# Kernel tuning notes

Hardware: AMD Instinct MI355X
Metric: run time of the kernel (lower is better)

## Reference

```python
import jax, jax.numpy as jnp
import numpy as np

B, NN, BBX, CLS, LAT = 8192, 64, 6, 16, 128
IN = LAT + NN + CLS  # 208
NT = B * NN          # total nodes in batched graph
NE = 4_194_304       # random edges (avg degree 8)


def setup_inputs() -> dict:
    key = jax.random.key(0)
    ks = jax.random.split(key, 16)
    p = lambda i, sh: (jax.random.normal(ks[i], sh, dtype=jnp.float32) * 0.05)
    return {
        "embedding": jax.random.normal(ks[0], (B, IN), dtype=jnp.float32),
        "E": jax.random.randint(ks[1], (2, NE), 0, NT, dtype=jnp.int32),
        "refine_iter": 2,
        "W1": p(2, (IN, 128)), "b1": p(3, (128,)),
        "W2": p(4, (128, 128)), "b2": p(5, (128,)),
        "Wbbx": p(6, (128, NN * BBX)), "bbbx": p(7, (NN * BBX,)),
        "Wlbl": p(8, (128, NN)), "blbl": p(9, (NN,)),
        "Wedge": p(10, (128, NN * NN)), "bedge": p(11, (NN * NN,)),
        "Wcls": p(12, (128, CLS)), "bcls": p(13, (CLS,)),
        "Wg": p(14, (BBX, BBX)), "bg": p(15, (BBX,)),
    }


def _gcn(h, src, dst, Wg, bg):
    # PyG GCNConv with add_self_loops=True, bias: D^-1/2 (A+I) D^-1/2 (h W) + b
    deg = jax.ops.segment_sum(jnp.ones(src.shape, h.dtype), dst, num_segments=NT)
    dinv = jax.lax.rsqrt(deg)  # deg >= 1 thanks to self-loops
    norm = dinv[src] * dinv[dst]
    m = h @ Wg  # [NT, BBX]
    out = jax.ops.segment_sum(m[src] * norm[:, None], dst, num_segments=NT)
    return out + bg


def reference(embedding, E, refine_iter, W1, b1, W2, b2, Wbbx, bbbx,
              Wlbl, blbl, Wedge, bedge, Wcls, bcls, Wg, bg):
    sig = jax.nn.sigmoid
    x = sig(embedding @ W1 + b1)
    x = sig(x @ W2 + b2)
    x = sig(x @ W2 + b2)  # dense2 applied twice (shared weights), as in source
    x_bbx = sig(x @ Wbbx + bbbx).reshape(B, NN, BBX)
    x_lbl = sig(x @ Wlbl + blbl).reshape(B, NN, 1)
    x_edge = sig(x @ Wedge + bedge).reshape(B, NN, NN)
    class_pred = jax.nn.softmax(x @ Wcls + bcls, axis=-1)

    loops = jnp.arange(NT, dtype=E.dtype)
    src = jnp.concatenate([E[0], loops])
    dst = jnp.concatenate([E[1], loops])

    x_bbx_refined = x_bbx
    for _ in range(int(refine_iter)):
        x_masked = x_bbx_refined * x_lbl  # labels=None -> mask with x_lbl
        flat = x_masked.reshape(NT, BBX)
        corr = jax.nn.sigmoid(_gcn(flat, src, dst, Wg, bg))
        # NOTE: source adds correction to the MASKED features (faithful)
        x_bbx_refined = (flat + corr).reshape(B, NN, BBX)
    return (x_bbx, x_lbl, x_edge, class_pred, x_bbx_refined)
```

## Files before the change

### kernel.cpp

```cpp
#include <hip/hip_runtime.h>
#include <hip/hip_bf16.h>
#include <math.h>

#define B_      8192
#define IN_     208
#define INP_    224
#define H_      128
#define NN_     64
#define BBX_    6
#define CLS_    16
#define NT_     (B_*NN_)
#define NE_     4194304
#define NB_     256
#define BSH_    11
#define CH_     4096
#define CAP_    18432

typedef __attribute__((ext_vector_type(8))) short short8v;
typedef __attribute__((ext_vector_type(4))) float f32x4;
typedef __attribute__((ext_vector_type(2))) float f32x2;

__device__ __forceinline__ float sigmoidf_(float v){ return 1.0f/(1.0f+__expf(-v)); }
__device__ __forceinline__ unsigned f2bf_(float f){
  unsigned u = __float_as_uint(f);
  return (u + 0x7FFFu + ((u >> 16) & 1u)) >> 16;
}

#if defined(__has_builtin)
# if __has_builtin(__builtin_amdgcn_cvt_pk_fp8_f32) && __has_builtin(__builtin_amdgcn_cvt_pk_f32_fp8)
#  define HW_FP8 1
# endif
#endif
#ifndef HW_FP8
# define HW_FP8 0
#endif

#if !HW_FP8
__device__ __forceinline__ unsigned enc1_(float v){
  unsigned u = __float_as_uint(v);
  unsigned s = (u >> 31) << 7;
  unsigned a = u & 0x7FFFFFFFu;
  unsigned r8;
  if (a < 0x3D000000u) {
    int q = (int)rintf(__uint_as_float(a) * 512.0f);
    r8 = (unsigned)q;
  } else {
    unsigned r = a + 0x7FFFFu + ((a >> 20) & 1u);
    int eb = (int)(r >> 23) - 120;
    r8 = (eb > 15) ? 0x7Eu : (unsigned)((eb << 3) | ((r >> 20) & 7u));
  }
  return s | r8;
}
__device__ __forceinline__ float dec1_(unsigned b){
  unsigned m = b & 7u, e = (b >> 3) & 0xFu;
  float mag = e ? __uint_as_float(((e + 120u) << 23) | (m << 20))
               : (float)m * 0.001953125f;
  return (b & 0x80u) ? -mag : mag;
}
#endif

__device__ __forceinline__ uint2 enc6_(const float mm[6]){
  uint2 o;
#if HW_FP8
  int w0 = __builtin_amdgcn_cvt_pk_fp8_f32(mm[0], mm[1], 0, false);
  w0     = __builtin_amdgcn_cvt_pk_fp8_f32(mm[2], mm[3], w0, true);
  int w1 = __builtin_amdgcn_cvt_pk_fp8_f32(mm[4], mm[5], 0, false);
  o.x = (unsigned)w0; o.y = (unsigned)w1;
#else
  o.x = enc1_(mm[0]) | (enc1_(mm[1])<<8) | (enc1_(mm[2])<<16) | (enc1_(mm[3])<<24);
  o.y = enc1_(mm[4]) | (enc1_(mm[5])<<8);
#endif
  return o;
}
__device__ __forceinline__ void dec6_(uint2 w, float v[6]){
#if HW_FP8
  f32x2 a = __builtin_amdgcn_cvt_pk_f32_fp8(w.x, false);
  f32x2 b = __builtin_amdgcn_cvt_pk_f32_fp8(w.x, true);
  f32x2 c = __builtin_amdgcn_cvt_pk_f32_fp8(w.y, false);
  v[0]=a[0]; v[1]=a[1]; v[2]=b[0]; v[3]=b[1]; v[4]=c[0]; v[5]=c[1];
#else
  v[0]=dec1_(w.x & 255u); v[1]=dec1_((w.x>>8)&255u);
  v[2]=dec1_((w.x>>16)&255u); v[3]=dec1_(w.x>>24);
  v[4]=dec1_(w.y & 255u); v[5]=dec1_((w.y>>8)&255u);
#endif
}

__global__ __launch_bounds__(256) void prep_k(
    const float* __restrict__ We, unsigned short* __restrict__ WtE,
    const float* __restrict__ Wb, unsigned short* __restrict__ WtB,
    const float* __restrict__ W2, unsigned short* __restrict__ Wt2,
    const float* __restrict__ Wl, unsigned short* __restrict__ WtL,
    const float* __restrict__ W1, unsigned short* __restrict__ W1t,
    const float* __restrict__ Wc, unsigned short* __restrict__ WtC)
{
  __shared__ unsigned short tile[64][136];
  const int t = threadIdx.x;
  if (blockIdx.x >= 73) {
    const int i = (blockIdx.x - 73) * 256 + t;
    if (i < H_ * INP_) {
      const int n = i / INP_, k = i % INP_;
      W1t[i] = (k < IN_) ? (unsigned short)f2bf_(W1[(size_t)k * H_ + n]) : 0;
    } else if (i < H_ * INP_ + CLS_ * H_) {
      const int j = i - H_ * INP_;
      const int n = j >> 7, k = j & 127;
      WtC[j] = (unsigned short)f2bf_(Wc[(size_t)k * CLS_ + n]);
    }
    return;
  }
  const float* W; unsigned short* Wt; int N, n0;
  if (blockIdx.x < 64)      { W = We; Wt = WtE; N = 4096; n0 = blockIdx.x * 64; }
  else if (blockIdx.x < 70) { W = Wb; Wt = WtB; N = 384;  n0 = (blockIdx.x-64) * 64; }
  else if (blockIdx.x < 72) { W = W2; Wt = Wt2; N = 128;  n0 = (blockIdx.x-70) * 64; }
  else                      { W = Wl; Wt = WtL; N = 64;   n0 = 0; }
  const int kk = t >> 6;
  const int nn = t & 63;
  for (int k0 = 0; k0 < 128; k0 += 4)
    tile[nn][k0 + kk] = (unsigned short)f2bf_(W[(size_t)(k0 + kk) * N + n0 + nn]);
  __syncthreads();
  const int rr = t >> 2, c0 = (t & 3) * 32;
  ushort4* dst = reinterpret_cast<ushort4*>(Wt + (size_t)(n0 + rr) * 128 + c0);
  #pragma unroll
  for (int q = 0; q < 8; ++q) {
    ushort4 o;
    o.x = tile[rr][c0 + q*4 + 0]; o.y = tile[rr][c0 + q*4 + 1];
    o.z = tile[rr][c0 + q*4 + 2]; o.w = tile[rr][c0 + q*4 + 3];
    dst[q] = o;
  }
}

__global__ __launch_bounds__(256) void fused_trunk_k(
    const float* __restrict__ emb,
    const unsigned short* __restrict__ W1t,
    const float* __restrict__ b1,
    const unsigned short* __restrict__ W2t,
    const float* __restrict__ b2,
    const unsigned short* __restrict__ WtL,
    const float* __restrict__ blbl,
    const unsigned short* __restrict__ WtC,
    const float* __restrict__ bcls,
    unsigned short* __restrict__ Xb,
    float* __restrict__ o_lbl, float* __restrict__ o_cls)
{
  __shared__ unsigned short s[64][136];
  const int tid  = threadIdx.x;
  const int wave = tid >> 6, lane = tid & 63;
  const int wm = wave >> 1, wn = wave & 1;
  const int r = lane & 15, g = lane >> 4;
  const int colB0 = wn * 64;
  const int grow0 = blockIdx.x * 64;

  f32x4 acc[2][4];
  short8v a[2], b[4];

  #pragma unroll
  for (int i = 0; i < 2; ++i)
    #pragma unroll
    for (int j = 0; j < 4; ++j)
      acc[i][j] = (f32x4){0.f, 0.f, 0.f, 0.f};

  for (int ks = 0; ks < INP_/32; ++ks) {
    const int koff = ks * 32 + g * 8;
    #pragma unroll
    for (int i = 0; i < 2; ++i) {
      if (koff < IN_) {
        const float* src = emb + (size_t)(grow0 + wm*32 + i*16 + r) * IN_ + koff;
        float4 v0 = *reinterpret_cast<const float4*>(src);
        float4 v1 = *reinterpret_cast<const float4*>(src + 4);
        a[i][0]=(short)f2bf_(v0.x); a[i][1]=(short)f2bf_(v0.y);
        a[i][2]=(short)f2bf_(v0.z); a[i][3]=(short)f2bf_(v0.w);
        a[i][4]=(short)f2bf_(v1.x); a[i][5]=(short)f2bf_(v1.y);
        a[i][6]=(short)f2bf_(v1.z); a[i][7]=(short)f2bf_(v1.w);
      } else {
        a[i] = (short8v){0,0,0,0,0,0,0,0};
      }
    }
    #pragma unroll
    for (int j = 0; j < 4; ++j)
      b[j] = *reinterpret_cast<const short8v*>(W1t + (size_t)(colB0 + j*16 + r) * INP_ + koff);
    #pragma unroll
    for (int i = 0; i < 2; ++i)
      #pragma unroll
      for (int j = 0; j < 4; ++j)
        acc[i][j] = __builtin_amdgcn_mfma_f32_16x16x32_bf16(a[i], b[j], acc[i][j], 0, 0, 0);
  }
  #pragma unroll
  for (int j = 0; j < 4; ++j) {
    const int col = colB0 + j*16 + r;
    const float bc = b1[col];
    #pragma unroll
    for (int i = 0; i < 2; ++i)
      #pragma unroll
      for (int q = 0; q < 4; ++q)
        s[wm*32 + i*16 + g*4 + q][col] = (unsigned short)f2bf_(sigmoidf_(acc[i][j][q] + bc));
  }
  __syncthreads();

  for (int layer = 0; layer < 2; ++layer) {
    #pragma unroll
    for (int i = 0; i < 2; ++i)
      #pragma unroll
      for (int j = 0; j < 4; ++j)
        acc[i][j] = (f32x4){0.f, 0.f, 0.f, 0.f};

    #pragma unroll
    for (int ks = 0; ks < 4; ++ks) {
      const int koff = ks * 32 + g * 8;
      #pragma unroll
      for (int i = 0; i < 2; ++i)
        a[i] = *reinterpret_cast<const short8v*>(&s[wm*32 + i*16 + r][koff]);
      #pragma unroll
      for (int j = 0; j < 4; ++j)
        b[j] = *reinterpret_cast<const short8v*>(W2t + (size_t)(colB0 + j*16 + r) * H_ + koff);
      #pragma unroll
      for (int i = 0; i < 2; ++i)
        #pragma unroll
        for (int j = 0; j < 4; ++j)
          acc[i][j] = __builtin_amdgcn_mfma_f32_16x16x32_bf16(a[i], b[j], acc[i][j], 0, 0, 0);
    }
    __syncthreads();

    #pragma unroll
    for (int j = 0; j < 4; ++j) {
      const int col = colB0 + j*16 + r;
      const float bc = b2[col];
      #pragma unroll
      for (int i = 0; i < 2; ++i) {
        #pragma unroll
        for (int q = 0; q < 4; ++q) {
          const float v = sigmoidf_(acc[i][j][q] + bc);
          const unsigned short vb = (unsigned short)f2bf_(v);
          s[wm*32 + i*16 + g*4 + q][col] = vb;
          if (layer == 1)
            Xb[(size_t)(grow0 + wm*32 + i*16 + g*4 + q) * H_ + col] = vb;
        }
      }
    }
    __syncthreads();
  }

  {
    f32x4 accl[4];
    #pragma unroll
    for (int j = 0; j < 4; ++j) accl[j] = (f32x4){0.f, 0.f, 0.f, 0.f};
    #pragma unroll
    for (int ks = 0; ks < 4; ++ks) {
      const int koff = ks * 32 + g * 8;
      const short8v av = *reinterpret_cast<const short8v*>(&s[wave*16 + r][koff]);
      #pragma unroll
      for (int j = 0; j < 4; ++j) {
        const short8v bv = *reinterpret_cast<const short8v*>(WtL + (size_t)(j*16 + r) * H_ + koff);
        accl[j] = __builtin_amdgcn_mfma_f32_16x16x32_bf16(av, bv, accl[j], 0, 0, 0);
      }
    }
    #pragma unroll
    for (int j = 0; j < 4; ++j) {
      const int col = j*16 + r;
      const float bc = blbl[col];
      #pragma unroll
      for (int q = 0; q < 4; ++q) {
        const int row = grow0 + wave*16 + g*4 + q;
        o_lbl[(size_t)row * NN_ + col] = sigmoidf_(accl[j][q] + bc);
      }
    }
  }

  {
    f32x4 accc = (f32x4){0.f, 0.f, 0.f, 0.f};
    #pragma unroll
    for (int ks = 0; ks < 4; ++ks) {
      const int koff = ks * 32 + g * 8;
      const short8v av = *reinterpret_cast<const short8v*>(&s[wave*16 + r][koff]);
      const short8v bv = *reinterpret_cast<const short8v*>(WtC + (size_t)r * H_ + koff);
      accc = __builtin_amdgcn_mfma_f32_16x16x32_bf16(av, bv, accc, 0, 0, 0);
    }
    const float bc = bcls[r];
    #pragma unroll
    for (int q = 0; q < 4; ++q) {
      float v = accc[q] + bc;
      float mx = v;
      for (int off = 8; off; off >>= 1) mx = fmaxf(mx, __shfl_xor(mx, off, 16));
      const float e = __expf(v - mx);
      float sm = e;
      for (int off = 8; off; off >>= 1) sm += __shfl_xor(sm, off, 16);
      const int row = grow0 + wave*16 + g*4 + q;
      o_cls[(size_t)row * CLS_ + r] = e / sm;
    }
  }
}

__global__ __launch_bounds__(256) void gemm_mfma_head(
    const unsigned short* __restrict__ Xb,
    const unsigned short* __restrict__ Wt,
    const float* __restrict__ bias, float* __restrict__ C, int N)
{
  const int tid  = threadIdx.x;
  const int wave = tid >> 6, lane = tid & 63;
  const int wm = wave >> 1, wn = wave & 1;
  const int r = lane & 15, g = lane >> 4;
  const int rowA0 = blockIdx.y * 128 + wm * 64;
  const int colB0 = blockIdx.x * 128 + wn * 64;

  f32x4 acc[4][4];
  #pragma unroll
  for (int i = 0; i < 4; ++i)
    #pragma unroll
    for (int j = 0; j < 4; ++j)
      acc[i][j] = (f32x4){0.f, 0.f, 0.f, 0.f};

  #pragma unroll
  for (int ks = 0; ks < 4; ++ks) {
    const int koff = ks * 32 + g * 8;
    short8v a[4], b[4];
    #pragma unroll
    for (int i = 0; i < 4; ++i)
      a[i] = *reinterpret_cast<const short8v*>(Xb + (size_t)(rowA0 + i*16 + r) * 128 + koff);
    #pragma unroll
    for (int j = 0; j < 4; ++j)
      b[j] = *reinterpret_cast<const short8v*>(Wt + (size_t)(colB0 + j*16 + r) * 128 + koff);
    #pragma unroll
    for (int i = 0; i < 4; ++i)
      #pragma unroll
      for (int j = 0; j < 4; ++j)
        acc[i][j] = __builtin_amdgcn_mfma_f32_16x16x32_bf16(a[i], b[j], acc[i][j], 0, 0, 0);
  }

  #pragma unroll
  for (int j = 0; j < 4; ++j) {
    const int col = colB0 + j*16 + r;
    const float bc = bias[col];
    #pragma unroll
    for (int i = 0; i < 4; ++i) {
      const int row0 = rowA0 + i*16 + g*4;
      #pragma unroll
      for (int q = 0; q < 4; ++q)
        C[(size_t)(row0 + q) * N + col] = sigmoidf_(acc[i][j][q] + bc);
    }
  }
}

__global__ __launch_bounds__(256) void binA_k(const int* __restrict__ E,
                                              int* __restrict__ gcnt,
                                              unsigned* __restrict__ binned) {
  __shared__ unsigned stage[CH_];
  __shared__ unsigned char stb[CH_];
  __shared__ int hist[NB_], lbase[NB_], gbase[NB_];
  const int t = threadIdx.x;
  const int e0 = blockIdx.x * CH_;

  hist[t] = 0;
  __syncthreads();

  unsigned pk[CH_/256];
  int rb[CH_/256];
  #pragma unroll
  for (int i = 0; i < CH_/256; ++i) {
    const int e = e0 + i * 256 + t;
    const int s = E[e];
    const unsigned d = (unsigned)E[NE_ + e];
    const int b = d >> BSH_;
    pk[i] = (unsigned)s | ((d & 2047u) << 19);
    rb[i] = atomicAdd(&hist[b], 1) | (b << 20);
  }
  __syncthreads();

  const int v = hist[t];
  lbase[t] = v; __syncthreads();
  #pragma unroll
  for (int off = 1; off < NB_; off <<= 1) {
    int x = (t >= off) ? lbase[t - off] : 0;
    __syncthreads();
    lbase[t] += x;
    __syncthreads();
  }
  const int excl = lbase[t] - v;
  __syncthreads();
  lbase[t] = excl;
  gbase[t] = t * CAP_ + atomicAdd(&gcnt[t], v);
  __syncthreads();

  #pragma unroll
  for (int i = 0; i < CH_/256; ++i) {
    const int b = rb[i] >> 20;
    const int pos = lbase[b] + (rb[i] & 0xFFFFF);
    stage[pos] = pk[i];
    stb[pos] = (unsigned char)b;
  }
  __syncthreads();

  for (int i = t; i < CH_; i += 256) {
    const int b = stb[i];
    const int tgt = gbase[b] + (i - lbase[b]);
    if (tgt < (b + 1) * CAP_)
      binned[tgt] = stage[i];
  }
}

__global__ __launch_bounds__(1024) void csr_k(const int* __restrict__ gcnt,
                                              const unsigned* __restrict__ binned,
                                              int* __restrict__ rowptr, int* __restrict__ cnt_g,
                                              float* __restrict__ dinv, int* __restrict__ csr_src) {
  __shared__ int cnt[2048];
  __shared__ int sd[1024];
  const int t = threadIdx.x, b = blockIdx.x;
  const int beg = b * CAP_;
  const int end = beg + min(gcnt[b], CAP_);

  cnt[t] = 0; cnt[t + 1024] = 0;
  __syncthreads();
  for (int i = beg + t; i < end; i += 1024)
    atomicAdd(&cnt[binned[i] >> 19], 1);
  __syncthreads();

  const int c0 = cnt[2 * t], c1 = cnt[2 * t + 1];
  const int s = c0 + c1;
  sd[t] = s; __syncthreads();
  #pragma unroll
  for (int off = 1; off < 1024; off <<= 1) {
    int x = (t >= off) ? sd[t - off] : 0;
    __syncthreads();
    sd[t] += x;
    __syncthreads();
  }
  const int excl = sd[t] - s;

  const int node0 = b * 2048 + 2 * t;
  rowptr[node0]     = beg + excl;
  rowptr[node0 + 1] = beg + excl + c0;
  cnt_g[node0]      = c0;
  cnt_g[node0 + 1]  = c1;
  dinv[node0]       = rsqrtf(1.0f + (float)c0);
  dinv[node0 + 1]   = rsqrtf(1.0f + (float)c1);
  __syncthreads();
  cnt[2 * t] = excl;
  cnt[2 * t + 1] = excl + c0;
  __syncthreads();

  for (int i = beg + t; i < end; i += 1024) {
    const unsigned pk = binned[i];
    const int dl = pk >> 19;
    const int slot = atomicAdd(&cnt[dl], 1);
    csr_src[beg + slot] = (int)(pk & 0x7FFFFu);
  }
}

__global__ __launch_bounds__(256) void gcn_pre_k(
    const float* __restrict__ refined, const float* __restrict__ lbl,
    const float* __restrict__ Wg, const float* __restrict__ dinv,
    uint2* __restrict__ ms8)
{
  int i = blockIdx.x * 256 + threadIdx.x;
  if (i >= NT_) return;
  float l = lbl[i];
  float di = dinv[i];
  float f[6];
  #pragma unroll
  for (int j = 0; j < 6; ++j) f[j] = refined[(size_t)i * 6 + j] * l;
  float mm[6];
  #pragma unroll
  for (int j = 0; j < 6; ++j) {
    float acc = 0.f;
    #pragma unroll
    for (int k = 0; k < 6; ++k) acc = fmaf(f[k], Wg[k * 6 + j], acc);
    mm[j] = acc * di;
  }
  ms8[i] = enc6_(mm);
}

template<int WRITE_MS>
__global__ __launch_bounds__(256) void gcn_gather_k(
    const float* __restrict__ rin, float* __restrict__ rout,
    const float* __restrict__ lbl,
    const uint2* __restrict__ ms8_in, uint2* __restrict__ ms8_out,
    const float* __restrict__ dinv,
    const int* __restrict__ rowptr, const int* __restrict__ cnt,
    const int* __restrict__ csr_src, const float* __restrict__ bg,
    const float* __restrict__ Wg)
{
  int i = blockIdx.x * 256 + threadIdx.x;
  if (i >= NT_) return;
  const float di = dinv[i];
  const float l  = lbl[i];
  const int beg = rowptr[i];
  const int kend = beg + cnt[i];

  float acc[6];
  dec6_(ms8_in[i], acc);

  int k = beg;
  for (; k + 7 < kend; k += 8) {
    int s_[8];
    uint2 w_[8];
    #pragma unroll
    for (int u = 0; u < 8; ++u) s_[u] = csr_src[k + u];
    #pragma unroll
    for (int u = 0; u < 8; ++u) w_[u] = ms8_in[s_[u]];
    #pragma unroll
    for (int u = 0; u < 8; ++u) {
      float v[6];
      dec6_(w_[u], v);
      #pragma unroll
      for (int j = 0; j < 6; ++j) acc[j] += v[j];
    }
  }
  for (; k + 3 < kend; k += 4) {
    const int s0 = csr_src[k],   s1 = csr_src[k+1];
    const int s2 = csr_src[k+2], s3 = csr_src[k+3];
    const uint2 w0 = ms8_in[s0], w1 = ms8_in[s1];
    const uint2 w2 = ms8_in[s2], w3 = ms8_in[s3];
    float v0[6], v1[6], v2[6], v3[6];
    dec6_(w0, v0); dec6_(w1, v1); dec6_(w2, v2); dec6_(w3, v3);
    #pragma unroll
    for (int j = 0; j < 6; ++j) acc[j] += (v0[j] + v1[j]) + (v2[j] + v3[j]);
  }
  for (; k < kend; ++k) {
    float v[6];
    dec6_(ms8_in[csr_src[k]], v);
    #pragma unroll
    for (int j = 0; j < 6; ++j) acc[j] += v[j];
  }

  float nr[6];
  #pragma unroll
  for (int j = 0; j < 6; ++j) {
    const float flat = rin[(size_t)i * 6 + j] * l;
    nr[j] = flat + sigmoidf_(di * acc[j] + bg[j]);
    rout[(size_t)i * 6 + j] = nr[j];
  }

  if (WRITE_MS) {
    float f[6], mm[6];
    #pragma unroll
    for (int j = 0; j < 6; ++j) f[j] = nr[j] * l;
    #pragma unroll
    for (int j = 0; j < 6; ++j) {
      float a = 0.f;
      #pragma unroll
      for (int kk = 0; kk < 6; ++kk) a = fmaf(f[kk], Wg[kk * 6 + j], a);
      mm[j] = a * di;
    }
    ms8_out[i] = enc6_(mm);
  }
}

extern "C" void kernel_launch(void* const* d_in, const int* in_sizes, int n_in,
                              void* d_out, int out_size, void* d_ws, size_t ws_size,
                              hipStream_t stream)
{
  const float* emb   = (const float*)d_in[0];
  const int*   E     = (const int*)  d_in[1];
  const float* W1    = (const float*)d_in[3];
  const float* b1    = (const float*)d_in[4];
  const float* W2    = (const float*)d_in[5];
  const float* b2    = (const float*)d_in[6];
  const float* Wbbx  = (const float*)d_in[7];
  const float* bbbx  = (const float*)d_in[8];
  const float* Wlbl  = (const float*)d_in[9];
  const float* blbl  = (const float*)d_in[10];
  const float* Wedge = (const float*)d_in[11];
  const float* bedge = (const float*)d_in[12];
  const float* Wcls  = (const float*)d_in[13];
  const float* bcls  = (const float*)d_in[14];
  const float* Wg    = (const float*)d_in[15];
  const float* bg    = (const float*)d_in[16];

  float* out    = (float*)d_out;
  float* o_bbx  = out;
  float* o_lbl  = out + 3145728;
  float* o_edge = out + 3670016;
  float* o_cls  = out + 37224448;
  float* o_ref  = out + 37355520;

  char* wsb = (char*)d_ws;
  unsigned short* WtL  = (unsigned short*)wsb;
  unsigned short* WtC  = WtL + (size_t)NN_ * H_;
  float* dinv    = (float*)(wsb + (size_t)1024 * 1024);
  int*   cnt_g   = (int*)(dinv + NT_);
  int*   rowptr  = cnt_g + NT_;
  int*   csr_src = rowptr + NT_;
  char*  U       = (char*)(csr_src + (size_t)NB_ * CAP_);
  unsigned*       binned = (unsigned*)U;
  unsigned short* Xb   = (unsigned short*)U;
  unsigned short* W1t  = Xb  + (size_t)B_ * H_;
  unsigned short* W2t  = W1t + (size_t)H_ * INP_;
  unsigned short* Wt_e = W2t + (size_t)H_ * H_;
  unsigned short* Wt_b = Wt_e + (size_t)4096 * H_;
  uint2*          ms8A = (uint2*)(Wt_b + (size_t)384 * H_);
  uint2*          ms8B = ms8A + NT_;
  int*            gcnt = (int*)(U + (size_t)NB_ * CAP_ * 4);

  hipMemsetAsync(gcnt, 0, NB_ * sizeof(int), stream);
  binA_k<<<NE_/CH_, 256, 0, stream>>>(E, gcnt, binned);
  csr_k <<<NB_, 1024, 0, stream>>>(gcnt, binned, rowptr, cnt_g, dinv, csr_src);

  prep_k<<<73 + (H_*INP_ + CLS_*H_ + 255)/256, 256, 0, stream>>>(
      Wedge, Wt_e, Wbbx, Wt_b, W2, W2t, Wlbl, WtL, W1, W1t, Wcls, WtC);

  fused_trunk_k<<<B_/64, 256, 0, stream>>>(emb, W1t, b1, W2t, b2,
                                           WtL, blbl, WtC, bcls, Xb, o_lbl, o_cls);

  gemm_mfma_head<<<dim3(4096/128, B_/128), 256, 0, stream>>>(Xb, Wt_e, bedge, o_edge, 4096);
  gemm_mfma_head<<<dim3(384/128,  B_/128), 256, 0, stream>>>(Xb, Wt_b, bbbx,  o_bbx,  384);

  gcn_pre_k<<<NT_/256, 256, 0, stream>>>(o_bbx, o_lbl, Wg, dinv, ms8A);
  gcn_gather_k<1><<<NT_/256, 256, 0, stream>>>(o_bbx, o_ref, o_lbl, ms8A, ms8B,
                                               dinv, rowptr, cnt_g, csr_src, bg, Wg);
  gcn_gather_k<0><<<NT_/256, 256, 0, stream>>>(o_ref, o_ref, o_lbl, ms8B, nullptr,
                                               dinv, rowptr, cnt_g, csr_src, bg, Wg);
}
```

Before: 219.7 us.

## Merge binning with weight prep and overlap edge-head GEMM with final GCN gather

```diff
diff --git a/kernel.cpp b/kernel.cpp
--- a/kernel.cpp
+++ b/kernel.cpp
@@ -15,6 +15,7 @@
 #define BSH_    11
 #define CH_     4096
 #define CAP_    18432
+#define GB_     (NT_/256)
 
 typedef __attribute__((ext_vector_type(8))) short short8v;
 typedef __attribute__((ext_vector_type(4))) float f32x4;
@@ -85,7 +86,8 @@
 #endif
 }
 
-__global__ __launch_bounds__(256) void prep_k(
+__global__ __launch_bounds__(256) void binprep_k(
+    const int* __restrict__ E, int* __restrict__ gcnt, unsigned* __restrict__ binned,
     const float* __restrict__ We, unsigned short* __restrict__ WtE,
     const float* __restrict__ Wb, unsigned short* __restrict__ WtB,
     const float* __restrict__ W2, unsigned short* __restrict__ Wt2,
@@ -93,38 +95,143 @@
     const float* __restrict__ W1, unsigned short* __restrict__ W1t,
     const float* __restrict__ Wc, unsigned short* __restrict__ WtC)
 {
-  __shared__ unsigned short tile[64][136];
+  __shared__ char smem[23552];
   const int t = threadIdx.x;
-  if (blockIdx.x >= 73) {
-    const int i = (blockIdx.x - 73) * 256 + t;
-    if (i < H_ * INP_) {
-      const int n = i / INP_, k = i % INP_;
-      W1t[i] = (k < IN_) ? (unsigned short)f2bf_(W1[(size_t)k * H_ + n]) : 0;
-    } else if (i < H_ * INP_ + CLS_ * H_) {
-      const int j = i - H_ * INP_;
-      const int n = j >> 7, k = j & 127;
-      WtC[j] = (unsigned short)f2bf_(Wc[(size_t)k * CLS_ + n]);
+
+  if (blockIdx.x >= 1024) {
+    const int pb = blockIdx.x - 1024;
+    if (pb >= 73) {
+      const int i = (pb - 73) * 256 + t;
+      if (i < H_ * INP_) {
+        const int n = i / INP_, k = i % INP_;
+        W1t[i] = (k < IN_) ? (unsigned short)f2bf_(W1[(size_t)k * H_ + n]) : 0;
+      } else if (i < H_ * INP_ + CLS_ * H_) {
+        const int j = i - H_ * INP_;
+        const int n = j >> 7, k = j & 127;
+        WtC[j] = (unsigned short)f2bf_(Wc[(size_t)k * CLS_ + n]);
+      }
+      return;
+    }
+    unsigned short (*tile)[136] = (unsigned short(*)[136])smem;
+    const float* W; unsigned short* Wt; int N, n0;
+    if (pb < 64)      { W = We; Wt = WtE; N = 4096; n0 = pb * 64; }
+    else if (pb < 70) { W = Wb; Wt = WtB; N = 384;  n0 = (pb-64) * 64; }
+    else if (pb < 72) { W = W2; Wt = Wt2; N = 128;  n0 = (pb-70) * 64; }
+    else              { W = Wl; Wt = WtL; N = 64;   n0 = 0; }
+    const int kk = t >> 6, nn = t & 63;
+    for (int k0 = 0; k0 < 128; k0 += 4)
+      tile[nn][k0 + kk] = (unsigned short)f2bf_(W[(size_t)(k0 + kk) * N + n0 + nn]);
+    __syncthreads();
+    const int rr = t >> 2, c0 = (t & 3) * 32;
+    ushort4* dst = reinterpret_cast<ushort4*>(Wt + (size_t)(n0 + rr) * 128 + c0);
+    #pragma unroll
+    for (int q = 0; q < 8; ++q) {
+      ushort4 o;
+      o.x = tile[rr][c0 + q*4 + 0]; o.y = tile[rr][c0 + q*4 + 1];
+      o.z = tile[rr][c0 + q*4 + 2]; o.w = tile[rr][c0 + q*4 + 3];
+      dst[q] = o;
     }
     return;
   }
-  const float* W; unsigned short* Wt; int N, n0;
-  if (blockIdx.x < 64)      { W = We; Wt = WtE; N = 4096; n0 = blockIdx.x * 64; }
-  else if (blockIdx.x < 70) { W = Wb; Wt = WtB; N = 384;  n0 = (blockIdx.x-64) * 64; }
-  else if (blockIdx.x < 72) { W = W2; Wt = Wt2; N = 128;  n0 = (blockIdx.x-70) * 64; }
-  else                      { W = Wl; Wt = WtL; N = 64;   n0 = 0; }
-  const int kk = t >> 6;
-  const int nn = t & 63;
-  for (int k0 = 0; k0 < 128; k0 += 4)
-    tile[nn][k0 + kk] = (unsigned short)f2bf_(W[(size_t)(k0 + kk) * N + n0 + nn]);
-  __syncthreads();
-  const int rr = t >> 2, c0 = (t & 3) * 32;
-  ushort4* dst = reinterpret_cast<ushort4*>(Wt + (size_t)(n0 + rr) * 128 + c0);
-  #pragma unroll
-  for (int q = 0; q < 8; ++q) {
-    ushort4 o;
-    o.x = tile[rr][c0 + q*4 + 0]; o.y = tile[rr][c0 + q*4 + 1];
-    o.z = tile[rr][c0 + q*4 + 2]; o.w = tile[rr][c0 + q*4 + 3];
-    dst[q] = o;
+
+  unsigned* stage = (unsigned*)smem;
+  unsigned char* stb = (unsigned char*)(smem + 16384);
+  int* hist  = (int*)(smem + 20480);
+  int* lbase = (int*)(smem + 21504);
+  int* gbase = (int*)(smem + 22528);
+  const int e0 = blockIdx.x * CH_;
+
+  hist[t] = 0;
+  __syncthreads();
+
+  unsigned pk[CH_/256];
+  int rb[CH_/256];
+  #pragma unroll
+  for (int i = 0; i < CH_/256; ++i) {
+    const int e = e0 + i * 256 + t;
+    const int s = E[e];
+    const unsigned d = (unsigned)E[NE_ + e];
+    const int b = d >> BSH_;
+    pk[i] = (unsigned)s | ((d & 2047u) << 19);
+    rb[i] = atomicAdd(&hist[b], 1) | (b << 20);
+  }
+  __syncthreads();
+
+  const int v = hist[t];
+  lbase[t] = v; __syncthreads();
+  #pragma unroll
+  for (int off = 1; off < NB_; off <<= 1) {
+    int x = (t >= off) ? lbase[t - off] : 0;
+    __syncthreads();
+    lbase[t] += x;
+    __syncthreads();
+  }
+  const int excl = lbase[t] - v;
+  __syncthreads();
+  lbase[t] = excl;
+  gbase[t] = t * CAP_ + atomicAdd(&gcnt[t], v);
+  __syncthreads();
+
+  #pragma unroll
+  for (int i = 0; i < CH_/256; ++i) {
+    const int b = rb[i] >> 20;
+    const int pos = lbase[b] + (rb[i] & 0xFFFFF);
+    stage[pos] = pk[i];
+    stb[pos] = (unsigned char)b;
+  }
+  __syncthreads();
+
+  for (int i = t; i < CH_; i += 256) {
+    const int b = stb[i];
+    const int tgt = gbase[b] + (i - lbase[b]);
+    if (tgt < (b + 1) * CAP_)
+      binned[tgt] = stage[i];
+  }
+}
+
+__global__ __launch_bounds__(1024) void csr_k(const int* __restrict__ gcnt,
+                                              const unsigned* __restrict__ binned,
+                                              int2* __restrict__ rowcnt,
+                                              float* __restrict__ dinv, int* __restrict__ csr_src) {
+  __shared__ int cnt[2048];
+  __shared__ int sd[1024];
+  const int t = threadIdx.x, b = blockIdx.x;
+  const int beg = b * CAP_;
+  const int end = beg + min(gcnt[b], CAP_);
+
+  cnt[t] = 0; cnt[t + 1024] = 0;
+  __syncthreads();
+  for (int i = beg + t; i < end; i += 1024)
+    atomicAdd(&cnt[binned[i] >> 19], 1);
+  __syncthreads();
+
+  const int c0 = cnt[2 * t], c1 = cnt[2 * t + 1];
+  const int s = c0 + c1;
+  sd[t] = s; __syncthreads();
+  #pragma unroll
+  for (int off = 1; off < 1024; off <<= 1) {
+    int x = (t >= off) ? sd[t - off] : 0;
+    __syncthreads();
+    sd[t] += x;
+    __syncthreads();
+  }
+  const int excl = sd[t] - s;
+
+  const int node0 = b * 2048 + 2 * t;
+  rowcnt[node0]     = make_int2(beg + excl, c0);
+  rowcnt[node0 + 1] = make_int2(beg + excl + c0, c1);
+  dinv[node0]       = rsqrtf(1.0f + (float)c0);
+  dinv[node0 + 1]   = rsqrtf(1.0f + (float)c1);
+  __syncthreads();
+  cnt[2 * t] = excl;
+  cnt[2 * t + 1] = excl + c0;
+  __syncthreads();
+
+  for (int i = beg + t; i < end; i += 1024) {
+    const unsigned pk = binned[i];
+    const int dl = pk >> 19;
+    const int slot = atomicAdd(&cnt[dl], 1);
+    csr_src[beg + slot] = (int)(pk & 0x7FFFFu);
   }
 }
 
@@ -338,111 +445,6 @@
   }
 }
 
-__global__ __launch_bounds__(256) void binA_k(const int* __restrict__ E,
-                                              int* __restrict__ gcnt,
-                                              unsigned* __restrict__ binned) {
-  __shared__ unsigned stage[CH_];
-  __shared__ unsigned char stb[CH_];
-  __shared__ int hist[NB_], lbase[NB_], gbase[NB_];
-  const int t = threadIdx.x;
-  const int e0 = blockIdx.x * CH_;
-
-  hist[t] = 0;
-  __syncthreads();
-
-  unsigned pk[CH_/256];
-  int rb[CH_/256];
-  #pragma unroll
-  for (int i = 0; i < CH_/256; ++i) {
-    const int e = e0 + i * 256 + t;
-    const int s = E[e];
-    const unsigned d = (unsigned)E[NE_ + e];
-    const int b = d >> BSH_;
-    pk[i] = (unsigned)s | ((d & 2047u) << 19);
-    rb[i] = atomicAdd(&hist[b], 1) | (b << 20);
-  }
-  __syncthreads();
-
-  const int v = hist[t];
-  lbase[t] = v; __syncthreads();
-  #pragma unroll
-  for (int off = 1; off < NB_; off <<= 1) {
-    int x = (t >= off) ? lbase[t - off] : 0;
-    __syncthreads();
-    lbase[t] += x;
-    __syncthreads();
-  }
-  const int excl = lbase[t] - v;
-  __syncthreads();
-  lbase[t] = excl;
-  gbase[t] = t * CAP_ + atomicAdd(&gcnt[t], v);
-  __syncthreads();
-
-  #pragma unroll
-  for (int i = 0; i < CH_/256; ++i) {
-    const int b = rb[i] >> 20;
-    const int pos = lbase[b] + (rb[i] & 0xFFFFF);
-    stage[pos] = pk[i];
-    stb[pos] = (unsigned char)b;
-  }
-  __syncthreads();
-
-  for (int i = t; i < CH_; i += 256) {
-    const int b = stb[i];
-    const int tgt = gbase[b] + (i - lbase[b]);
-    if (tgt < (b + 1) * CAP_)
-      binned[tgt] = stage[i];
-  }
-}
-
-__global__ __launch_bounds__(1024) void csr_k(const int* __restrict__ gcnt,
-                                              const unsigned* __restrict__ binned,
-                                              int* __restrict__ rowptr, int* __restrict__ cnt_g,
-                                              float* __restrict__ dinv, int* __restrict__ csr_src) {
-  __shared__ int cnt[2048];
-  __shared__ int sd[1024];
-  const int t = threadIdx.x, b = blockIdx.x;
-  const int beg = b * CAP_;
-  const int end = beg + min(gcnt[b], CAP_);
-
-  cnt[t] = 0; cnt[t + 1024] = 0;
-  __syncthreads();
-  for (int i = beg + t; i < end; i += 1024)
-    atomicAdd(&cnt[binned[i] >> 19], 1);
-  __syncthreads();
-
-  const int c0 = cnt[2 * t], c1 = cnt[2 * t + 1];
-  const int s = c0 + c1;
-  sd[t] = s; __syncthreads();
-  #pragma unroll
-  for (int off = 1; off < 1024; off <<= 1) {
-    int x = (t >= off) ? sd[t - off] : 0;
-    __syncthreads();
-    sd[t] += x;
-    __syncthreads();
-  }
-  const int excl = sd[t] - s;
-
-  const int node0 = b * 2048 + 2 * t;
-  rowptr[node0]     = beg + excl;
-  rowptr[node0 + 1] = beg + excl + c0;
-  cnt_g[node0]      = c0;
-  cnt_g[node0 + 1]  = c1;
-  dinv[node0]       = rsqrtf(1.0f + (float)c0);
-  dinv[node0 + 1]   = rsqrtf(1.0f + (float)c1);
-  __syncthreads();
-  cnt[2 * t] = excl;
-  cnt[2 * t + 1] = excl + c0;
-  __syncthreads();
-
-  for (int i = beg + t; i < end; i += 1024) {
-    const unsigned pk = binned[i];
-    const int dl = pk >> 19;
-    const int slot = atomicAdd(&cnt[dl], 1);
-    csr_src[beg + slot] = (int)(pk & 0x7FFFFu);
-  }
-}
-
 __global__ __launch_bounds__(256) void gcn_pre_k(
     const float* __restrict__ refined, const float* __restrict__ lbl,
     const float* __restrict__ Wg, const float* __restrict__ dinv,
@@ -467,41 +469,25 @@
 }
 
 template<int WRITE_MS>
-__global__ __launch_bounds__(256) void gcn_gather_k(
+__device__ __forceinline__ void gather_body(
+    int i,
     const float* __restrict__ rin, float* __restrict__ rout,
     const float* __restrict__ lbl,
     const uint2* __restrict__ ms8_in, uint2* __restrict__ ms8_out,
     const float* __restrict__ dinv,
-    const int* __restrict__ rowptr, const int* __restrict__ cnt,
-    const int* __restrict__ csr_src, const float* __restrict__ bg,
-    const float* __restrict__ Wg)
-{
-  int i = blockIdx.x * 256 + threadIdx.x;
-  if (i >= NT_) return;
+    const int2* __restrict__ rowcnt, const int* __restrict__ csr_src,
+    const float* __restrict__ bg, const float* __restrict__ Wg)
+{
   const float di = dinv[i];
   const float l  = lbl[i];
-  const int beg = rowptr[i];
-  const int kend = beg + cnt[i];
+  const int2 rc = rowcnt[i];
+  const int beg = rc.x;
+  const int kend = beg + rc.y;
 
   float acc[6];
   dec6_(ms8_in[i], acc);
 
   int k = beg;
-  for (; k + 7 < kend; k += 8) {
-    int s_[8];
-    uint2 w_[8];
-    #pragma unroll
-    for (int u = 0; u < 8; ++u) s_[u] = csr_src[k + u];
-    #pragma unroll
-    for (int u = 0; u < 8; ++u) w_[u] = ms8_in[s_[u]];
-    #pragma unroll
-    for (int u = 0; u < 8; ++u) {
-      float v[6];
-      dec6_(w_[u], v);
-      #pragma unroll
-      for (int j = 0; j < 6; ++j) acc[j] += v[j];
-    }
-  }
   for (; k + 3 < kend; k += 4) {
     const int s0 = csr_src[k],   s1 = csr_src[k+1];
     const int s2 = csr_src[k+2], s3 = csr_src[k+3];
@@ -539,6 +525,80 @@
       mm[j] = a * di;
     }
     ms8_out[i] = enc6_(mm);
+  }
+}
+
+__global__ __launch_bounds__(256) void gcn_gather1_k(
+    const float* __restrict__ rin, float* __restrict__ rout,
+    const float* __restrict__ lbl,
+    const uint2* __restrict__ ms8_in, uint2* __restrict__ ms8_out,
+    const float* __restrict__ dinv,
+    const int2* __restrict__ rowcnt, const int* __restrict__ csr_src,
+    const float* __restrict__ bg, const float* __restrict__ Wg)
+{
+  const int i = blockIdx.x * 256 + threadIdx.x;
+  gather_body<1>(i, rin, rout, lbl, ms8_in, ms8_out, dinv, rowcnt, csr_src, bg, Wg);
+}
+
+__global__ __launch_bounds__(256) void tail_k(
+    float* __restrict__ o_ref, const float* __restrict__ lbl,
+    const uint2* __restrict__ ms8_in,
+    const float* __restrict__ dinv,
+    const int2* __restrict__ rowcnt, const int* __restrict__ csr_src,
+    const float* __restrict__ bg, const float* __restrict__ Wg,
+    const unsigned short* __restrict__ Xb, const unsigned short* __restrict__ WtE,
+    const float* __restrict__ bedge, float* __restrict__ o_edge)
+{
+  if (blockIdx.x < GB_) {
+    const int i = blockIdx.x * 256 + threadIdx.x;
+    gather_body<0>(i, o_ref, o_ref, lbl, ms8_in, nullptr, dinv, rowcnt, csr_src, bg, Wg);
+    return;
+  }
+  const int bx = blockIdx.x - GB_;
+  const int tm = bx >> 6;
+  const int tn = bx & 63;
+  const int tid  = threadIdx.x;
+  const int wave = tid >> 6, lane = tid & 63;
+  const int wm = wave >> 1, wn = wave & 1;
+  const int r = lane & 15, g = lane >> 4;
+  const int row0 = tm * 64 + wm * 32;
+  const int col0 = tn * 64 + wn * 32;
+
+  f32x4 acc[2][2];
+  #pragma unroll
+  for (int i = 0; i < 2; ++i)
+    #pragma unroll
+    for (int j = 0; j < 2; ++j)
+      acc[i][j] = (f32x4){0.f, 0.f, 0.f, 0.f};
+
+  #pragma unroll
+  for (int ks = 0; ks < 4; ++ks) {
+    const int koff = ks * 32 + g * 8;
+    short8v a[2], b[2];
+    #pragma unroll
+    for (int i = 0; i < 2; ++i)
+      a[i] = *reinterpret_cast<const short8v*>(Xb + (size_t)(row0 + i*16 + r) * 128 + koff);
+    #pragma unroll
+    for (int j = 0; j < 2; ++j)
+      b[j] = *reinterpret_cast<const short8v*>(WtE + (size_t)(col0 + j*16 + r) * 128 + koff);
+    #pragma unroll
+    for (int i = 0; i < 2; ++i)
+      #pragma unroll
+      for (int j = 0; j < 2; ++j)
+        acc[i][j] = __builtin_amdgcn_mfma_f32_16x16x32_bf16(a[i], b[j], acc[i][j], 0, 0, 0);
+  }
+
+  #pragma unroll
+  for (int j = 0; j < 2; ++j) {
+    const int col = col0 + j*16 + r;
+    const float bc = bedge[col];
+    #pragma unroll
+    for (int i = 0; i < 2; ++i) {
+      const int rr0 = row0 + i*16 + g*4;
+      #pragma unroll
+      for (int q = 0; q < 4; ++q)
+        o_edge[(size_t)(rr0 + q) * 4096 + col] = sigmoidf_(acc[i][j][q] + bc);
+    }
   }
 }
 
@@ -573,37 +633,31 @@
   char* wsb = (char*)d_ws;
   unsigned short* WtL  = (unsigned short*)wsb;
   unsigned short* WtC  = WtL + (size_t)NN_ * H_;
-  float* dinv    = (float*)(wsb + (size_t)1024 * 1024);
-  int*   cnt_g   = (int*)(dinv + NT_);
-  int*   rowptr  = cnt_g + NT_;
-  int*   csr_src = rowptr + NT_;
-  char*  U       = (char*)(csr_src + (size_t)NB_ * CAP_);
-  unsigned*       binned = (unsigned*)U;
-  unsigned short* Xb   = (unsigned short*)U;
-  unsigned short* W1t  = Xb  + (size_t)B_ * H_;
+  unsigned short* W1t  = WtC + (size_t)CLS_ * H_;
   unsigned short* W2t  = W1t + (size_t)H_ * INP_;
   unsigned short* Wt_e = W2t + (size_t)H_ * H_;
   unsigned short* Wt_b = Wt_e + (size_t)4096 * H_;
-  uint2*          ms8A = (uint2*)(Wt_b + (size_t)384 * H_);
-  uint2*          ms8B = ms8A + NT_;
-  int*            gcnt = (int*)(U + (size_t)NB_ * CAP_ * 4);
+  unsigned short* Xb   = Wt_b + (size_t)384 * H_;
+  float* dinv    = (float*)(Xb + (size_t)B_ * H_);
+  int2*  rowcnt  = (int2*)(dinv + NT_);
+  int*   csr_src = (int*)(rowcnt + NT_);
+  char*  U       = (char*)(csr_src + (size_t)NB_ * CAP_);
+  unsigned* binned = (unsigned*)U;
+  uint2* ms8A    = (uint2*)U;
+  uint2* ms8B    = ms8A + NT_;
+  int*   gcnt    = (int*)(U + (size_t)NB_ * CAP_ * 4);
 
   hipMemsetAsync(gcnt, 0, NB_ * sizeof(int), stream);
-  binA_k<<<NE_/CH_, 256, 0, stream>>>(E, gcnt, binned);
-  csr_k <<<NB_, 1024, 0, stream>>>(gcnt, binned, rowptr, cnt_g, dinv, csr_src);
-
-  prep_k<<<73 + (H_*INP_ + CLS_*H_ + 255)/256, 256, 0, stream>>>(
+  binprep_k<<<1024 + 73 + (H_*INP_ + CLS_*H_ + 255)/256, 256, 0, stream>>>(
+      E, gcnt, binned,
       Wedge, Wt_e, Wbbx, Wt_b, W2, W2t, Wlbl, WtL, W1, W1t, Wcls, WtC);
-
+  csr_k<<<NB_, 1024, 0, stream>>>(gcnt, binned, rowcnt, dinv, csr_src);
   fused_trunk_k<<<B_/64, 256, 0, stream>>>(emb, W1t, b1, W2t, b2,
                                            WtL, blbl, WtC, bcls, Xb, o_lbl, o_cls);
-
-  gemm_mfma_head<<<dim3(4096/128, B_/128), 256, 0, stream>>>(Xb, Wt_e, bedge, o_edge, 4096);
-  gemm_mfma_head<<<dim3(384/128,  B_/128), 256, 0, stream>>>(Xb, Wt_b, bbbx,  o_bbx,  384);
-
+  gemm_mfma_head<<<dim3(384/128, B_/128), 256, 0, stream>>>(Xb, Wt_b, bbbx, o_bbx, 384);
   gcn_pre_k<<<NT_/256, 256, 0, stream>>>(o_bbx, o_lbl, Wg, dinv, ms8A);
-  gcn_gather_k<1><<<NT_/256, 256, 0, stream>>>(o_bbx, o_ref, o_lbl, ms8A, ms8B,
-                                               dinv, rowptr, cnt_g, csr_src, bg, Wg);
-  gcn_gather_k<0><<<NT_/256, 256, 0, stream>>>(o_ref, o_ref, o_lbl, ms8B, nullptr,
-                                               dinv, rowptr, cnt_g, csr_src, bg, Wg);
-}
+  gcn_gather1_k<<<GB_, 256, 0, stream>>>(o_bbx, o_ref, o_lbl, ms8A, ms8B,
+                                         dinv, rowcnt, csr_src, bg, Wg);
+  tail_k<<<GB_ + 8192, 256, 0, stream>>>(o_ref, o_lbl, ms8B, dinv, rowcnt, csr_src,
+                                         bg, Wg, Xb, Wt_e, bedge, o_edge);
+}
```

New measurement: 240.1 us. 9.3% more time.
